# Kernel tuning notes

Hardware: AMD Instinct MI355X
Metric: run time of the kernel (lower is better)

## Reference

```python
import jax, jax.numpy as jnp
import numpy as np

IN_FEATURES = 512
DIM_EXPLOSION = 20
OUT_FEATURES = IN_FEATURES * DIM_EXPLOSION  # 10240
NB_PROJ_ENTRIES = 6
HASH_LENGTH = 32
BATCH = 4096


def _make_sparse_proj(key):
    """Sparse binary random projection: each of the OUT_FEATURES rows has
    NB_PROJ_ENTRIES entries set to 1 (as in OlfactoryModel.create_rand_proj_matrix)."""
    idx = jax.random.randint(key, (OUT_FEATURES, NB_PROJ_ENTRIES), 0, IN_FEATURES)
    rows = jnp.arange(OUT_FEATURES)[:, None]
    W = jnp.zeros((OUT_FEATURES, IN_FEATURES), dtype=jnp.float32)
    return W.at[rows, idx].set(1.0)


def setup_inputs() -> dict:
    key = jax.random.key(0)
    k1, k2 = jax.random.split(key)
    inp = jax.random.uniform(k1, (BATCH, IN_FEATURES), dtype=jnp.float32)
    W = _make_sparse_proj(k2)
    return {"input": inp, "weight": W, "hash_length": HASH_LENGTH}


def reference(input, weight, hash_length):
    # F.linear: [B, in] @ [out, in]^T -> [B, out]
    x = jnp.einsum('bi,oi->bo', input, weight)
    # MB_sparsify: winner-take-all, keep top `hash_length` activations per row, zero the rest
    topv = jax.lax.top_k(x, hash_length)[0]          # [B, k]
    thresh = topv[:, -1:]                            # k-th largest per row
    return jnp.where(x >= thresh, x, jnp.zeros_like(x))
```

## Files before the change

kernel.cpp:

```cpp
#include <hip/hip_runtime.h>


typedef float f4 __attribute__((ext_vector_type(4)));

constexpr int IN_F   = 512;
constexpr int OUT_F  = 10240;
constexpr int TPB    = 512;
constexpr int ROWS   = 4;
constexpr int FPT    = OUT_F / TPB;
constexpr int NBINS  = 1024;
constexpr int CHUNK  = 8;
constexpr int NCHUNK = NBINS / CHUNK;
constexpr int NWAVES = TPB / 64;

static_assert(ROWS * NCHUNK == TPB, "scan assumes one chunk per thread");

__global__ __launch_bounds__(256) void extract_idx(const float* __restrict__ W,
                                                   uint4* __restrict__ packed,
                                                   int out_f) {
  int row  = blockIdx.x * 4 + (threadIdx.x >> 6);
  int lane = threadIdx.x & 63;
  if (row >= out_f) return;

  const float* wr = W + (size_t)row * IN_F;
  unsigned long long masks[8];
#pragma unroll
  for (int c = 0; c < 8; ++c) {
    float v = wr[c * 64 + lane];
    masks[c] = __ballot(v != 0.0f);
  }
  if (lane == 0) {
    unsigned idx[6] = {IN_F, IN_F, IN_F, IN_F, IN_F, IN_F};
    int n = 0;
#pragma unroll
    for (int c = 0; c < 8; ++c) {
      unsigned long long m = masks[c];
      while (m && n < 6) {
        int b = __builtin_ctzll(m);
        idx[n++] = (unsigned)(c * 64 + b);
        m &= m - 1;
      }
    }
    uint4 r;
    r.x = idx[0] | (idx[1] << 16);
    r.y = idx[2] | (idx[3] << 16);
    r.z = idx[4] | (idx[5] << 16);
    r.w = (unsigned)n;
    packed[row] = r;
  }
}

__global__ __launch_bounds__(TPB, 4) void fly_hash(const float* __restrict__ inp,
                                                   const uint4* __restrict__ packed,
                                                   const int* __restrict__ kptr,
                                                   float* __restrict__ out) {
  __shared__ f4  in4[IN_F + 1];
  __shared__ int hist[ROWS * NBINS];
  __shared__ int csum[TPB];
  __shared__ int wsum[NWAVES][ROWS];
  __shared__ int sh_bstar[ROWS];

  const int tid  = threadIdx.x;
  const int row0 = blockIdx.x * ROWS;
  const int k    = *kptr;

  {
    const float* p = inp + (size_t)row0 * IN_F + tid;
    f4 v;
    v.x = p[0];
    v.y = p[IN_F];
    v.z = p[2 * IN_F];
    v.w = p[3 * IN_F];
    in4[tid] = v;
  }
  if (tid == 0) { f4 z = {0.0f, 0.0f, 0.0f, 0.0f}; in4[IN_F] = z; }
  if (tid < ROWS) sh_bstar[tid] = -1;
  for (int i = tid; i < ROWS * NBINS; i += TPB) hist[i] = 0;
  __syncthreads();

  f4 x4[FPT];
#pragma unroll
  for (int i = 0; i < FPT; ++i) {
    uint4 r = packed[tid + i * TPB];
    f4 s = in4[r.x & 0xFFFFu];
    s += in4[r.x >> 16];
    s += in4[r.y & 0xFFFFu];
    s += in4[r.y >> 16];
    s += in4[r.z & 0xFFFFu];
    s += in4[r.z >> 16];
    x4[i] = s;
#pragma unroll
    for (int r2 = 0; r2 < ROWS; ++r2) {
      float v = (r2 == 0) ? s.x : (r2 == 1) ? s.y : (r2 == 2) ? s.z : s.w;
      if (v >= 4.0f) {
        int b = (int)((v - 4.0f) * 512.0f);
        b = b > NBINS - 1 ? NBINS - 1 : b;
        atomicAdd(&hist[r2 * NBINS + b], 1);
      }
    }
  }
  __syncthreads();

  {
    const int r = tid >> 7;
    const int c = tid & (NCHUNK - 1);
    const int base = r * NBINS + c * CHUNK;
    int ssum = 0;
#pragma unroll
    for (int j = 0; j < CHUNK; ++j) ssum += hist[base + j];
    csum[tid] = ssum;
    __syncthreads();
    for (int st = 1; st < NCHUNK; st <<= 1) {
      int v = csum[tid] + ((c + st < NCHUNK) ? csum[tid + st] : 0);
      __syncthreads();
      csum[tid] = v;
      __syncthreads();
    }
    int above = (c + 1 < NCHUNK) ? csum[tid + 1] : 0;
    if (csum[tid] >= k && above < k) {
      int acc = above;
      int bsel = c * CHUNK;
      for (int b = c * CHUNK + CHUNK - 1; b >= c * CHUNK; --b) {
        acc += hist[r * NBINS + b];
        if (acc >= k) { bsel = b; break; }
      }
      sh_bstar[r] = bsel;
    }
  }
  __syncthreads();

  unsigned lo[ROWS], hi[ROWS];
#pragma unroll
  for (int r = 0; r < ROWS; ++r) {
    int b = sh_bstar[r];
    if (b < 0) {
      lo[r] = 0u;
      hi[r] = __float_as_uint(4.0f + (1.0f / 512.0f));
    } else {
      lo[r] = __float_as_uint(4.0f + (float)b * (1.0f / 512.0f));
      hi[r] = __float_as_uint(4.0f + (float)(b + 1) * (1.0f / 512.0f));
    }
  }
  const int lane = tid & 63;
  const int wid  = tid >> 6;
  while (lo[0] < hi[0] || lo[1] < hi[1] || lo[2] < hi[2] || lo[3] < hi[3]) {
    unsigned mid[ROWS];
    float fm[ROWS];
#pragma unroll
    for (int r = 0; r < ROWS; ++r) {
      mid[r] = lo[r] + ((hi[r] - lo[r] + 1u) >> 1);
      fm[r] = __uint_as_float(mid[r]);
    }
    int c0 = 0, c1 = 0, c2 = 0, c3 = 0;
#pragma unroll
    for (int i = 0; i < FPT; ++i) {
      c0 += (int)__popcll(__ballot(x4[i].x >= fm[0]));
      c1 += (int)__popcll(__ballot(x4[i].y >= fm[1]));
      c2 += (int)__popcll(__ballot(x4[i].z >= fm[2]));
      c3 += (int)__popcll(__ballot(x4[i].w >= fm[3]));
    }
    if (lane == 0) {
      wsum[wid][0] = c0; wsum[wid][1] = c1; wsum[wid][2] = c2; wsum[wid][3] = c3;
    }
    __syncthreads();
    int tot[ROWS] = {0, 0, 0, 0};
#pragma unroll
    for (int w = 0; w < NWAVES; ++w)
#pragma unroll
      for (int r = 0; r < ROWS; ++r) tot[r] += wsum[w][r];
#pragma unroll
    for (int r = 0; r < ROWS; ++r) {
      if (lo[r] < hi[r]) {
        if (tot[r] >= k) lo[r] = mid[r]; else hi[r] = mid[r] - 1u;
      }
    }
    __syncthreads();
  }
  const float t0 = __uint_as_float(lo[0]);
  const float t1 = __uint_as_float(lo[1]);
  const float t2 = __uint_as_float(lo[2]);
  const float t3 = __uint_as_float(lo[3]);

  float* o0 = out + (size_t)(row0 + 0) * OUT_F;
  float* o1 = out + (size_t)(row0 + 1) * OUT_F;
  float* o2 = out + (size_t)(row0 + 2) * OUT_F;
  float* o3 = out + (size_t)(row0 + 3) * OUT_F;
#pragma unroll
  for (int i = 0; i < FPT; ++i) {
    int f = tid + i * TPB;
    f4 v = x4[i];
    o0[f] = (v.x >= t0) ? v.x : 0.0f;
    o1[f] = (v.y >= t1) ? v.y : 0.0f;
    o2[f] = (v.z >= t2) ? v.z : 0.0f;
    o3[f] = (v.w >= t3) ? v.w : 0.0f;
  }
}

extern "C" void kernel_launch(void* const* d_in, const int* in_sizes, int n_in,
                              void* d_out, int out_size, void* d_ws, size_t ws_size,
                              hipStream_t stream) {
  const float* inp = (const float*)d_in[0];
  const float* W   = (const float*)d_in[1];
  const int* kptr  = (const int*)d_in[2];
  float* out       = (float*)d_out;

  const int batch = in_sizes[0] / IN_F;
  const int out_f = in_sizes[1] / IN_F;

  uint4* packed = (uint4*)d_ws;

  hipLaunchKernelGGL(extract_idx, dim3((out_f + 3) / 4), dim3(256), 0, stream,
                     W, packed, out_f);
  hipLaunchKernelGGL(fly_hash, dim3(batch / ROWS), dim3(TPB), 0, stream,
                     inp, packed, kptr, out);
}
```

Baseline: 283.0 us.

## Resolve top-k threshold by ranking threshold-bin candidates, halve rows per block

Instead of always running a bitwise binary search over the threshold bin with block-wide ballots and barriers, values that fall in the selected histogram bin are collected into a small shared list. When that list fits in 64 entries, one wave ranks the candidates directly to find the exact k-th value. The binary search stays as a fallback. The block now handles 2 rows instead of 4, which doubles the grid and lowers register pressure, and output writes use nontemporal stores. The cost is an extra pass over the values plus shared atomics, and each block does less work.

```diff
diff --git a/kernel.cpp b/kernel.cpp
--- a/kernel.cpp
+++ b/kernel.cpp
@@ -1,19 +1,18 @@
 #include <hip/hip_runtime.h>
 
 
-typedef float f4 __attribute__((ext_vector_type(4)));
+typedef float f2 __attribute__((ext_vector_type(2)));
 
 constexpr int IN_F   = 512;
 constexpr int OUT_F  = 10240;
 constexpr int TPB    = 512;
-constexpr int ROWS   = 4;
+constexpr int ROWS   = 2;
 constexpr int FPT    = OUT_F / TPB;
 constexpr int NBINS  = 1024;
 constexpr int CHUNK  = 8;
 constexpr int NCHUNK = NBINS / CHUNK;
 constexpr int NWAVES = TPB / 64;
-
-static_assert(ROWS * NCHUNK == TPB, "scan assumes one chunk per thread");
+constexpr int CAP    = 64;
 
 __global__ __launch_bounds__(256) void extract_idx(const float* __restrict__ W,
                                                    uint4* __restrict__ packed,
@@ -54,11 +53,14 @@
                                                    const uint4* __restrict__ packed,
                                                    const int* __restrict__ kptr,
                                                    float* __restrict__ out) {
-  __shared__ f4  in4[IN_F + 1];
-  __shared__ int hist[ROWS * NBINS];
-  __shared__ int csum[TPB];
-  __shared__ int wsum[NWAVES][ROWS];
-  __shared__ int sh_bstar[ROWS];
+  __shared__ f2    in2[IN_F + 1];
+  __shared__ int   hist[ROWS * NBINS];
+  __shared__ int   csum[ROWS * NCHUNK];
+  __shared__ int   wsum[NWAVES][ROWS];
+  __shared__ int   sh_bstar[ROWS], sh_above[ROWS], sh_n[ROWS], sh_cnt[ROWS];
+  __shared__ float sh_list[ROWS][CAP];
+  __shared__ float sh_thr[ROWS];
+  __shared__ int   sh_need[ROWS];
 
   const int tid  = threadIdx.x;
   const int row0 = blockIdx.x * ROWS;
@@ -66,65 +68,123 @@
 
   {
     const float* p = inp + (size_t)row0 * IN_F + tid;
-    f4 v;
+    f2 v;
     v.x = p[0];
     v.y = p[IN_F];
-    v.z = p[2 * IN_F];
-    v.w = p[3 * IN_F];
-    in4[tid] = v;
-  }
-  if (tid == 0) { f4 z = {0.0f, 0.0f, 0.0f, 0.0f}; in4[IN_F] = z; }
-  if (tid < ROWS) sh_bstar[tid] = -1;
+    in2[tid] = v;
+  }
+  if (tid == 0) { f2 z = {0.0f, 0.0f}; in2[IN_F] = z; }
+  if (tid < ROWS) { sh_bstar[tid] = -1; sh_cnt[tid] = 0; }
   for (int i = tid; i < ROWS * NBINS; i += TPB) hist[i] = 0;
   __syncthreads();
 
-  f4 x4[FPT];
+  f2 x2[FPT];
 #pragma unroll
   for (int i = 0; i < FPT; ++i) {
     uint4 r = packed[tid + i * TPB];
-    f4 s = in4[r.x & 0xFFFFu];
-    s += in4[r.x >> 16];
-    s += in4[r.y & 0xFFFFu];
-    s += in4[r.y >> 16];
-    s += in4[r.z & 0xFFFFu];
-    s += in4[r.z >> 16];
-    x4[i] = s;
-#pragma unroll
-    for (int r2 = 0; r2 < ROWS; ++r2) {
-      float v = (r2 == 0) ? s.x : (r2 == 1) ? s.y : (r2 == 2) ? s.z : s.w;
-      if (v >= 4.0f) {
-        int b = (int)((v - 4.0f) * 512.0f);
-        b = b > NBINS - 1 ? NBINS - 1 : b;
-        atomicAdd(&hist[r2 * NBINS + b], 1);
-      }
-    }
-  }
-  __syncthreads();
-
-  {
+    f2 s = in2[r.x & 0xFFFFu];
+    s += in2[r.x >> 16];
+    s += in2[r.y & 0xFFFFu];
+    s += in2[r.y >> 16];
+    s += in2[r.z & 0xFFFFu];
+    s += in2[r.z >> 16];
+    x2[i] = s;
+    if (s.x >= 4.0f) {
+      int b = (int)((s.x - 4.0f) * 512.0f);
+      b = b > NBINS - 1 ? NBINS - 1 : b;
+      atomicAdd(&hist[b], 1);
+    }
+    if (s.y >= 4.0f) {
+      int b = (int)((s.y - 4.0f) * 512.0f);
+      b = b > NBINS - 1 ? NBINS - 1 : b;
+      atomicAdd(&hist[NBINS + b], 1);
+    }
+  }
+  __syncthreads();
+
+  {
+    const bool active = tid < ROWS * NCHUNK;
     const int r = tid >> 7;
     const int c = tid & (NCHUNK - 1);
-    const int base = r * NBINS + c * CHUNK;
-    int ssum = 0;
-#pragma unroll
-    for (int j = 0; j < CHUNK; ++j) ssum += hist[base + j];
-    csum[tid] = ssum;
+    if (active) {
+      const int base = r * NBINS + c * CHUNK;
+      int ssum = 0;
+#pragma unroll
+      for (int j = 0; j < CHUNK; ++j) ssum += hist[base + j];
+      csum[tid] = ssum;
+    }
     __syncthreads();
     for (int st = 1; st < NCHUNK; st <<= 1) {
-      int v = csum[tid] + ((c + st < NCHUNK) ? csum[tid + st] : 0);
-      __syncthreads();
-      csum[tid] = v;
-      __syncthreads();
-    }
-    int above = (c + 1 < NCHUNK) ? csum[tid + 1] : 0;
-    if (csum[tid] >= k && above < k) {
-      int acc = above;
-      int bsel = c * CHUNK;
-      for (int b = c * CHUNK + CHUNK - 1; b >= c * CHUNK; --b) {
-        acc += hist[r * NBINS + b];
-        if (acc >= k) { bsel = b; break; }
-      }
-      sh_bstar[r] = bsel;
+      int v = 0;
+      if (active) v = csum[tid] + ((c + st < NCHUNK) ? csum[tid + st] : 0);
+      __syncthreads();
+      if (active) csum[tid] = v;
+      __syncthreads();
+    }
+    if (active) {
+      int above_chunk = (c + 1 < NCHUNK) ? csum[tid + 1] : 0;
+      if (csum[tid] >= k && above_chunk < k) {
+        int acc = above_chunk;
+        int bsel = c * CHUNK, abv = above_chunk;
+        for (int b = c * CHUNK + CHUNK - 1; b >= c * CHUNK; --b) {
+          int h = hist[r * NBINS + b];
+          if (acc + h >= k) { bsel = b; abv = acc; break; }
+          acc += h;
+        }
+        sh_bstar[r] = bsel;
+        sh_above[r] = abv;
+        sh_n[r]     = hist[r * NBINS + bsel];
+      }
+    }
+  }
+  __syncthreads();
+
+  {
+    const int b0 = sh_bstar[0], b1 = sh_bstar[1];
+#pragma unroll
+    for (int i = 0; i < FPT; ++i) {
+      f2 s = x2[i];
+      if (s.x >= 4.0f) {
+        int b = (int)((s.x - 4.0f) * 512.0f);
+        b = b > NBINS - 1 ? NBINS - 1 : b;
+        if (b == b0) {
+          int p = atomicAdd(&sh_cnt[0], 1);
+          if (p < CAP) sh_list[0][p] = s.x;
+        }
+      }
+      if (s.y >= 4.0f) {
+        int b = (int)((s.y - 4.0f) * 512.0f);
+        b = b > NBINS - 1 ? NBINS - 1 : b;
+        if (b == b1) {
+          int p = atomicAdd(&sh_cnt[1], 1);
+          if (p < CAP) sh_list[1][p] = s.y;
+        }
+      }
+    }
+  }
+  __syncthreads();
+
+  {
+    const int wid  = tid >> 6;
+    const int lane = tid & 63;
+    if (wid < ROWS) {
+      const int r = wid;
+      const int bst = sh_bstar[r];
+      const int n   = (bst >= 0) ? sh_n[r] : CAP + 1;
+      if (bst >= 0 && n <= CAP) {
+        const int j = k - sh_above[r];
+        float vl = (lane < n) ? sh_list[r][lane] : -1.0f;
+        int c_gt = 0, c_ge = 0;
+        for (int m = 0; m < n; ++m) {
+          float u = sh_list[r][m];
+          c_gt += (u > vl);
+          c_ge += (u >= vl);
+        }
+        if (lane < n && c_gt < j && c_ge >= j) sh_thr[r] = vl;
+        if (lane == 0) sh_need[r] = 0;
+      } else {
+        if (lane == 0) sh_need[r] = 1;
+      }
     }
   }
   __syncthreads();
@@ -132,67 +192,64 @@
   unsigned lo[ROWS], hi[ROWS];
 #pragma unroll
   for (int r = 0; r < ROWS; ++r) {
-    int b = sh_bstar[r];
-    if (b < 0) {
-      lo[r] = 0u;
-      hi[r] = __float_as_uint(4.0f + (1.0f / 512.0f));
+    if (sh_need[r]) {
+      int b = sh_bstar[r];
+      if (b < 0) {
+        lo[r] = 0u;
+        hi[r] = __float_as_uint(4.0f + (1.0f / 512.0f));
+      } else {
+        lo[r] = __float_as_uint(4.0f + (float)b * (1.0f / 512.0f));
+        hi[r] = __float_as_uint(4.0f + (float)(b + 1) * (1.0f / 512.0f));
+      }
     } else {
-      lo[r] = __float_as_uint(4.0f + (float)b * (1.0f / 512.0f));
-      hi[r] = __float_as_uint(4.0f + (float)(b + 1) * (1.0f / 512.0f));
-    }
-  }
-  const int lane = tid & 63;
-  const int wid  = tid >> 6;
-  while (lo[0] < hi[0] || lo[1] < hi[1] || lo[2] < hi[2] || lo[3] < hi[3]) {
-    unsigned mid[ROWS];
-    float fm[ROWS];
-#pragma unroll
-    for (int r = 0; r < ROWS; ++r) {
-      mid[r] = lo[r] + ((hi[r] - lo[r] + 1u) >> 1);
-      fm[r] = __uint_as_float(mid[r]);
-    }
-    int c0 = 0, c1 = 0, c2 = 0, c3 = 0;
-#pragma unroll
-    for (int i = 0; i < FPT; ++i) {
-      c0 += (int)__popcll(__ballot(x4[i].x >= fm[0]));
-      c1 += (int)__popcll(__ballot(x4[i].y >= fm[1]));
-      c2 += (int)__popcll(__ballot(x4[i].z >= fm[2]));
-      c3 += (int)__popcll(__ballot(x4[i].w >= fm[3]));
-    }
-    if (lane == 0) {
-      wsum[wid][0] = c0; wsum[wid][1] = c1; wsum[wid][2] = c2; wsum[wid][3] = c3;
-    }
-    __syncthreads();
-    int tot[ROWS] = {0, 0, 0, 0};
-#pragma unroll
-    for (int w = 0; w < NWAVES; ++w)
-#pragma unroll
-      for (int r = 0; r < ROWS; ++r) tot[r] += wsum[w][r];
-#pragma unroll
-    for (int r = 0; r < ROWS; ++r) {
-      if (lo[r] < hi[r]) {
-        if (tot[r] >= k) lo[r] = mid[r]; else hi[r] = mid[r] - 1u;
-      }
-    }
-    __syncthreads();
-  }
-  const float t0 = __uint_as_float(lo[0]);
-  const float t1 = __uint_as_float(lo[1]);
-  const float t2 = __uint_as_float(lo[2]);
-  const float t3 = __uint_as_float(lo[3]);
+      lo[r] = hi[r] = 0u;
+    }
+  }
+  {
+    const int lane = tid & 63;
+    const int wid  = tid >> 6;
+    while (lo[0] < hi[0] || lo[1] < hi[1]) {
+      unsigned mid[ROWS];
+      float fm[ROWS];
+#pragma unroll
+      for (int r = 0; r < ROWS; ++r) {
+        mid[r] = lo[r] + ((hi[r] - lo[r] + 1u) >> 1);
+        fm[r] = __uint_as_float(mid[r]);
+      }
+      int c0 = 0, c1 = 0;
+#pragma unroll
+      for (int i = 0; i < FPT; ++i) {
+        c0 += (int)__popcll(__ballot(x2[i].x >= fm[0]));
+        c1 += (int)__popcll(__ballot(x2[i].y >= fm[1]));
+      }
+      if (lane == 0) { wsum[wid][0] = c0; wsum[wid][1] = c1; }
+      __syncthreads();
+      int tot[ROWS] = {0, 0};
+#pragma unroll
+      for (int w = 0; w < NWAVES; ++w) {
+        tot[0] += wsum[w][0];
+        tot[1] += wsum[w][1];
+      }
+#pragma unroll
+      for (int r = 0; r < ROWS; ++r) {
+        if (lo[r] < hi[r]) {
+          if (tot[r] >= k) lo[r] = mid[r]; else hi[r] = mid[r] - 1u;
+        }
+      }
+      __syncthreads();
+    }
+  }
+  const float t0 = sh_need[0] ? __uint_as_float(lo[0]) : sh_thr[0];
+  const float t1 = sh_need[1] ? __uint_as_float(lo[1]) : sh_thr[1];
 
   float* o0 = out + (size_t)(row0 + 0) * OUT_F;
   float* o1 = out + (size_t)(row0 + 1) * OUT_F;
-  float* o2 = out + (size_t)(row0 + 2) * OUT_F;
-  float* o3 = out + (size_t)(row0 + 3) * OUT_F;
 #pragma unroll
   for (int i = 0; i < FPT; ++i) {
     int f = tid + i * TPB;
-    f4 v = x4[i];
-    o0[f] = (v.x >= t0) ? v.x : 0.0f;
-    o1[f] = (v.y >= t1) ? v.y : 0.0f;
-    o2[f] = (v.z >= t2) ? v.z : 0.0f;
-    o3[f] = (v.w >= t3) ? v.w : 0.0f;
+    f2 v = x2[i];
+    __builtin_nontemporal_store((v.x >= t0) ? v.x : 0.0f, &o0[f]);
+    __builtin_nontemporal_store((v.y >= t1) ? v.y : 0.0f, &o1[f]);
   }
 }
 
```

Result: faster. 248.2 us (-12.3%).
